# Kernel optimization log

Measured on AMD Instinct MI355X. Metric: run time of the kernel, lower is better.

The kernel has to match this reference:

```python
import jax, jax.numpy as jnp
import numpy as np

TEMPERATURE = 1.0


def setup_inputs() -> dict:
    key = jax.random.key(0)
    kq, kk, kv = jax.random.split(key, 3)
    shape = (2, 16, 2048, 64)  # B, H, L, D
    q = jax.random.normal(kq, shape, dtype=jnp.float32)
    k = jax.random.normal(kk, shape, dtype=jnp.float32)
    v = jax.random.normal(kv, shape, dtype=jnp.float32)
    return {"q": q, "k": k, "v": v}


def reference(q, k, v):
    # q, k, v: [B, H, L, D]
    L = q.shape[2]
    # scores: [B, H, L, L]; note: divided by temperature, NOT sqrt(D), per source
    scores = jnp.einsum("bhqd,bhkd->bhqk", q, k) / TEMPERATURE
    # causal mask: position j > i masked with -inf
    causal = jnp.tril(jnp.ones((L, L), dtype=bool))  # True = keep
    scores = jnp.where(causal, scores, -jnp.inf)
    attn = jax.nn.softmax(scores, axis=-1)
    out = jnp.einsum("bhqk,bhkd->bhqd", attn, v)
    return out
```

## Files before the change

### kernel.cpp

```cpp
#include <hip/hip_runtime.h>
#include <math.h>


typedef __attribute__((ext_vector_type(8))) _Float16 f16x8;
typedef __attribute__((ext_vector_type(4))) _Float16 f16x4;
typedef __attribute__((ext_vector_type(4))) float f32x4;
typedef unsigned short u16;
typedef __attribute__((ext_vector_type(8))) u16 u16x8;

constexpr int Lq = 2048;
constexpr int Dd = 64;
constexpr int KT = 64;
constexpr int BH = 32;

#define SWZB(row, bcol) ((((row) * 128) + (bcol)) ^ (((row) & 7) << 4))

#define GLOAD_LDS16(g, l)                                                     \
  __builtin_amdgcn_global_load_lds(                                           \
      (const __attribute__((address_space(1))) void*)(g),                     \
      (__attribute__((address_space(3))) void*)(l), 16, 0, 0)

static __device__ __forceinline__ u16 f2h(float x) {
  return __builtin_bit_cast(u16, (_Float16)x);
}

constexpr int PREP_KB = (BH * Lq * Dd) / (256 * 16);

__global__ __launch_bounds__(256)
void attn_prep(const float* __restrict__ K, const float* __restrict__ V,
               u16* __restrict__ Kh, u16* __restrict__ VTh) {
  const int b = blockIdx.x;
  const int tid = threadIdx.x;
  if (b < PREP_KB) {
    const size_t base = ((size_t)b * 256 + tid) * 16;
    const f32x4* src = reinterpret_cast<const f32x4*>(K + base);
    u16x8 o0, o1;
    #pragma unroll
    for (int i = 0; i < 2; ++i) {
      const f32x4 a = src[i];
      #pragma unroll
      for (int j = 0; j < 4; ++j) o0[i * 4 + j] = f2h(a[j]);
    }
    #pragma unroll
    for (int i = 0; i < 2; ++i) {
      const f32x4 a = src[2 + i];
      #pragma unroll
      for (int j = 0; j < 4; ++j) o1[i * 4 + j] = f2h(a[j]);
    }
    *reinterpret_cast<u16x8*>(Kh + base) = o0;
    *reinterpret_cast<u16x8*>(Kh + base + 8) = o1;
  } else {
    __shared__ u16 lt[64][66];
    const int vb = b - PREP_KB;
    const int h = vb >> 5, tt = vb & 31;
    const float* Vt = V + ((size_t)h * Lq + tt * 64) * Dd;
    const int r = tid & 63, dg = tid >> 6;
    #pragma unroll
    for (int i = 0; i < 4; ++i) {
      const f32x4 a = *reinterpret_cast<const f32x4*>(Vt + (size_t)r * Dd + dg * 16 + i * 4);
      #pragma unroll
      for (int j = 0; j < 2; ++j) {
        const unsigned two =
            (unsigned)f2h(a[2 * j]) | ((unsigned)f2h(a[2 * j + 1]) << 16);
        *reinterpret_cast<unsigned*>(&lt[r][dg * 16 + i * 4 + j * 2]) = two;
      }
    }
    __syncthreads();
    const int d = tid >> 2, kq = tid & 3;
    u16x8 w0, w1;
    #pragma unroll
    for (int j = 0; j < 8; ++j) w0[j] = lt[kq * 16 + j][d];
    #pragma unroll
    for (int j = 0; j < 8; ++j) w1[j] = lt[kq * 16 + 8 + j][d];
    u16* dst = VTh + ((size_t)h * Dd + d) * Lq + tt * 64 + kq * 16;
    *reinterpret_cast<u16x8*>(dst) = w0;
    *reinterpret_cast<u16x8*>(dst + 8) = w1;
  }
}

constexpr int THREADS = 512;
constexpr int CHUNK = 128;
constexpr int NCHUNK = Lq / CHUNK;
constexpr int PAIRS = NCHUNK / 2;

__global__ __launch_bounds__(THREADS)
void attn_main(const float* __restrict__ Q, float* __restrict__ O,
               const u16* __restrict__ Kh, const u16* __restrict__ VTh) {
  __shared__ char ks[2][8192];
  __shared__ char vt2[2][8192];
  __shared__ char pl[8][2048];

  const int tid  = threadIdx.x;
  const int lane = tid & 63;
  const int wv   = tid >> 6;
  const int l15  = lane & 15;
  const int g    = lane >> 4;

  const int bh = blockIdx.x / PAIRS;
  const int pr = blockIdx.x % PAIRS;
  const float* Qb = Q + (size_t)bh * Lq * Dd;
  float*       Ob = O + (size_t)bh * Lq * Dd;
  const u16*   Kb = Kh + (size_t)bh * Lq * Dd;
  const u16*   Vb = VTh + (size_t)bh * Dd * Lq;
  char* pw = pl[wv];

  const int lsw = lane ^ ((lane >> 3) & 7);
  const int r_ = lsw >> 3, s_ = lsw & 7;

  #pragma unroll 1
  for (int phase = 0; phase < 2; ++phase) {
    const int chunk = (phase == 0) ? pr : (NCHUNK - 1 - pr);
    const int row0  = chunk * CHUNK;
    const int T     = 2 * (chunk + 1);
    const int qrow  = row0 + wv * 16;
    const int tLast = qrow >> 6;

    f16x8 qf[2];
    #pragma unroll
    for (int kk = 0; kk < 2; ++kk) {
      const float* qp = Qb + (size_t)(qrow + l15) * Dd + kk * 32 + g * 8;
      const f32x4 a = *reinterpret_cast<const f32x4*>(qp);
      const f32x4 b = *reinterpret_cast<const f32x4*>(qp + 4);
      f16x8 q8;
      #pragma unroll
      for (int i = 0; i < 4; ++i) {
        q8[i]     = (_Float16)a[i];
        q8[i + 4] = (_Float16)b[i];
      }
      qf[kk] = q8;
    }

    float m[4], lsum[4];
    f32x4 o[4];
    #pragma unroll
    for (int r = 0; r < 4; ++r) { m[r] = -INFINITY; lsum[r] = 0.f; }
    #pragma unroll
    for (int nd = 0; nd < 4; ++nd) o[nd] = f32x4{0.f, 0.f, 0.f, 0.f};

    __syncthreads();
    GLOAD_LDS16(Kb + (size_t)(8 * wv) * Dd + lsw * 8, ks[0] + wv * 1024);
    GLOAD_LDS16(Vb + (size_t)(8 * wv + r_) * Lq + s_ * 8, vt2[0] + wv * 1024);

    int cur = 0;
    #pragma unroll 1
    for (int t = 0; t < T; ++t) {
      __syncthreads();
      if (t + 1 < T) {
        GLOAD_LDS16(Kb + (size_t)((t + 1) * KT + 8 * wv) * Dd + lsw * 8,
                    ks[cur ^ 1] + wv * 1024);
        GLOAD_LDS16(Vb + (size_t)(8 * wv + r_) * Lq + (t + 1) * KT + s_ * 8,
                    vt2[cur ^ 1] + wv * 1024);
      }
      if (t <= tLast) {
        const char* kb = ks[cur];
        const char* vb = vt2[cur];

        f32x4 s[4];
        #pragma unroll
        for (int n = 0; n < 4; ++n) s[n] = f32x4{0.f, 0.f, 0.f, 0.f};
        __builtin_amdgcn_s_setprio(1);
        #pragma unroll
        for (int kk = 0; kk < 2; ++kk) {
          #pragma unroll
          for (int n = 0; n < 4; ++n) {
            const f16x8 kf = *reinterpret_cast<const f16x8*>(
                kb + SWZB(n * 16 + l15, kk * 64 + g * 16));
            s[n] = __builtin_amdgcn_mfma_f32_16x16x32_f16(qf[kk], kf, s[n], 0, 0, 0);
          }
        }
        __builtin_amdgcn_s_setprio(0);

        if (t == tLast) {
          #pragma unroll
          for (int n = 0; n < 4; ++n) {
            const int key = t * KT + n * 16 + l15;
            #pragma unroll
            for (int r = 0; r < 4; ++r) {
              if (key > qrow + 4 * g + r) s[n][r] = -INFINITY;
            }
          }
        }

        float rmax[4], rsum[4], scale[4];
        #pragma unroll
        for (int r = 0; r < 4; ++r)
          rmax[r] = fmaxf(fmaxf(s[0][r], s[1][r]), fmaxf(s[2][r], s[3][r]));
        #pragma unroll
        for (int mk = 1; mk <= 8; mk <<= 1) {
          #pragma unroll
          for (int r = 0; r < 4; ++r)
            rmax[r] = fmaxf(rmax[r], __shfl_xor(rmax[r], mk));
        }
        #pragma unroll
        for (int r = 0; r < 4; ++r) {
          const float mn = fmaxf(m[r], rmax[r]);
          scale[r] = __expf(m[r] - mn);
          m[r] = mn;
        }
        #pragma unroll
        for (int n = 0; n < 4; ++n) {
          #pragma unroll
          for (int r = 0; r < 4; ++r) s[n][r] = __expf(s[n][r] - m[r]);
        }
        #pragma unroll
        for (int r = 0; r < 4; ++r)
          rsum[r] = (s[0][r] + s[1][r]) + (s[2][r] + s[3][r]);
        #pragma unroll
        for (int mk = 1; mk <= 8; mk <<= 1) {
          #pragma unroll
          for (int r = 0; r < 4; ++r) rsum[r] += __shfl_xor(rsum[r], mk);
        }
        #pragma unroll
        for (int r = 0; r < 4; ++r) lsum[r] = lsum[r] * scale[r] + rsum[r];
        #pragma unroll
        for (int nd = 0; nd < 4; ++nd) {
          #pragma unroll
          for (int r = 0; r < 4; ++r) o[nd][r] *= scale[r];
        }

        #pragma unroll
        for (int n = 0; n < 4; ++n) {
          #pragma unroll
          for (int r = 0; r < 4; ++r) {
            *reinterpret_cast<_Float16*>(
                pw + SWZB(4 * g + r, (n * 16 + l15) * 2)) = (_Float16)s[n][r];
          }
        }
        asm volatile("s_waitcnt lgkmcnt(0)" ::: "memory");
        __builtin_amdgcn_sched_barrier(0);

        __builtin_amdgcn_s_setprio(1);
        #pragma unroll
        for (int kblk = 0; kblk < 2; ++kblk) {
          const f16x8 pf = *reinterpret_cast<const f16x8*>(
              pw + SWZB(l15, kblk * 64 + g * 16));
          #pragma unroll
          for (int nd = 0; nd < 4; ++nd) {
            const f16x8 vf = *reinterpret_cast<const f16x8*>(
                vb + SWZB(nd * 16 + l15, kblk * 64 + g * 16));
            o[nd] = __builtin_amdgcn_mfma_f32_16x16x32_f16(pf, vf, o[nd], 0, 0, 0);
          }
        }
        __builtin_amdgcn_s_setprio(0);
      }
      cur ^= 1;
    }

    float inv[4];
    #pragma unroll
    for (int r = 0; r < 4; ++r) inv[r] = 1.f / lsum[r];
    #pragma unroll
    for (int nd = 0; nd < 4; ++nd) {
      #pragma unroll
      for (int r = 0; r < 4; ++r) {
        Ob[(size_t)(qrow + 4 * g + r) * Dd + nd * 16 + l15] = o[nd][r] * inv[r];
      }
    }
  }
}

__global__ __launch_bounds__(256)
void causal_attn_fb(const float* __restrict__ Q, const float* __restrict__ K,
                    const float* __restrict__ V, float* __restrict__ O) {
  __shared__ char ks[2][KT * 128];
  __shared__ char vt[2][Dd * 128];
  __shared__ char pl[4][16 * 128];
  const int tid = threadIdx.x, lane = tid & 63, wv = tid >> 6;
  const int l15 = lane & 15, g = lane >> 4;
  const int kg = tid & 15, dq = tid >> 4;
  const int bh = blockIdx.x / 16, pr = blockIdx.x % 16;
  const size_t base = (size_t)bh * Lq * Dd;
  const float* Qb = Q + base; const float* Kb = K + base;
  const float* Vb = V + base; float* Ob = O + base;
  char* pw = pl[wv];
  #pragma unroll 1
  for (int phase = 0; phase < 2; ++phase) {
    const int chunk = (phase == 0) ? pr : (31 - pr);
    const int row0 = chunk * 64, T = chunk + 1, qrow = row0 + wv * 16;
    f16x8 qf[2];
    #pragma unroll
    for (int kk = 0; kk < 2; ++kk) {
      const float* qp = Qb + (size_t)(qrow + l15) * Dd + kk * 32 + g * 8;
      const f32x4 a = *reinterpret_cast<const f32x4*>(qp);
      const f32x4 b = *reinterpret_cast<const f32x4*>(qp + 4);
      f16x8 q8;
      #pragma unroll
      for (int i = 0; i < 4; ++i) { q8[i] = (_Float16)a[i]; q8[i+4] = (_Float16)b[i]; }
      qf[kk] = q8;
    }
    float m[4], lsum[4]; f32x4 o[4];
    #pragma unroll
    for (int r = 0; r < 4; ++r) { m[r] = -INFINITY; lsum[r] = 0.f; }
    #pragma unroll
    for (int nd = 0; nd < 4; ++nd) o[nd] = f32x4{0.f, 0.f, 0.f, 0.f};
    {
      f32x4 kreg[4], vreg[4];
      #pragma unroll
      for (int i = 0; i < 4; ++i) {
        const int c = tid + i * 256;
        kreg[i] = *reinterpret_cast<const f32x4*>(Kb + (size_t)(c >> 4) * Dd + (c & 15) * 4);
      }
      #pragma unroll
      for (int c = 0; c < 4; ++c)
        vreg[c] = *reinterpret_cast<const f32x4*>(Vb + (size_t)(kg * 4 + c) * Dd + dq * 4);
      __syncthreads();
      #pragma unroll
      for (int i = 0; i < 4; ++i) {
        const int c = tid + i * 256;
        f16x4 h;
        #pragma unroll
        for (int j = 0; j < 4; ++j) h[j] = (_Float16)kreg[i][j];
        *reinterpret_cast<f16x4*>(ks[0] + SWZB(c >> 4, (c & 15) * 8)) = h;
      }
      #pragma unroll
      for (int j = 0; j < 4; ++j) {
        f16x4 h;
        #pragma unroll
        for (int c = 0; c < 4; ++c) h[c] = (_Float16)vreg[c][j];
        *reinterpret_cast<f16x4*>(vt[0] + SWZB(dq * 4 + j, kg * 8)) = h;
      }
    }
    int cur = 0;
    #pragma unroll 1
    for (int t = 0; t < T; ++t) {
      __syncthreads();
      const char* kb = ks[cur]; const char* vb = vt[cur];
      f32x4 kreg[4], vreg[4];
      const bool pfn = (t + 1 < T);
      if (pfn) {
        const float* Kt = Kb + (size_t)(t + 1) * KT * Dd;
        const float* Vt = Vb + (size_t)(t + 1) * KT * Dd;
        #pragma unroll
        for (int i = 0; i < 4; ++i) {
          const int c = tid + i * 256;
          kreg[i] = *reinterpret_cast<const f32x4*>(Kt + (size_t)(c >> 4) * Dd + (c & 15) * 4);
        }
        #pragma unroll
        for (int c = 0; c < 4; ++c)
          vreg[c] = *reinterpret_cast<const f32x4*>(Vt + (size_t)(kg * 4 + c) * Dd + dq * 4);
      }
      f32x4 s[4];
      #pragma unroll
      for (int n = 0; n < 4; ++n) s[n] = f32x4{0.f, 0.f, 0.f, 0.f};
      #pragma unroll
      for (int kk = 0; kk < 2; ++kk) {
        #pragma unroll
        for (int n = 0; n < 4; ++n) {
          const f16x8 kf = *reinterpret_cast<const f16x8*>(kb + SWZB(n * 16 + l15, kk * 64 + g * 16));
          s[n] = __builtin_amdgcn_mfma_f32_16x16x32_f16(qf[kk], kf, s[n], 0, 0, 0);
        }
      }
      if (t == T - 1) {
        #pragma unroll
        for (int n = 0; n < 4; ++n) {
          const int key = t * KT + n * 16 + l15;
          #pragma unroll
          for (int r = 0; r < 4; ++r)
            if (key > qrow + 4 * g + r) s[n][r] = -INFINITY;
        }
      }
      float rmax[4], rsum[4], scale[4];
      #pragma unroll
      for (int r = 0; r < 4; ++r)
        rmax[r] = fmaxf(fmaxf(s[0][r], s[1][r]), fmaxf(s[2][r], s[3][r]));
      #pragma unroll
      for (int mk = 1; mk <= 8; mk <<= 1) {
        #pragma unroll
        for (int r = 0; r < 4; ++r) rmax[r] = fmaxf(rmax[r], __shfl_xor(rmax[r], mk));
      }
      #pragma unroll
      for (int r = 0; r < 4; ++r) {
        const float mn = fmaxf(m[r], rmax[r]);
        scale[r] = __expf(m[r] - mn); m[r] = mn;
      }
      #pragma unroll
      for (int n = 0; n < 4; ++n) {
        #pragma unroll
        for (int r = 0; r < 4; ++r) s[n][r] = __expf(s[n][r] - m[r]);
      }
      #pragma unroll
      for (int r = 0; r < 4; ++r) rsum[r] = (s[0][r] + s[1][r]) + (s[2][r] + s[3][r]);
      #pragma unroll
      for (int mk = 1; mk <= 8; mk <<= 1) {
        #pragma unroll
        for (int r = 0; r < 4; ++r) rsum[r] += __shfl_xor(rsum[r], mk);
      }
      #pragma unroll
      for (int r = 0; r < 4; ++r) lsum[r] = lsum[r] * scale[r] + rsum[r];
      #pragma unroll
      for (int nd = 0; nd < 4; ++nd) {
        #pragma unroll
        for (int r = 0; r < 4; ++r) o[nd][r] *= scale[r];
      }
      #pragma unroll
      for (int n = 0; n < 4; ++n) {
        #pragma unroll
        for (int r = 0; r < 4; ++r)
          *reinterpret_cast<_Float16*>(pw + SWZB(4 * g + r, (n * 16 + l15) * 2)) = (_Float16)s[n][r];
      }
      asm volatile("s_waitcnt lgkmcnt(0)" ::: "memory");
      __builtin_amdgcn_sched_barrier(0);
      #pragma unroll
      for (int kblk = 0; kblk < 2; ++kblk) {
        const f16x8 pf = *reinterpret_cast<const f16x8*>(pw + SWZB(l15, kblk * 64 + g * 16));
        #pragma unroll
        for (int nd = 0; nd < 4; ++nd) {
          const f16x8 vf = *reinterpret_cast<const f16x8*>(vb + SWZB(nd * 16 + l15, kblk * 64 + g * 16));
          o[nd] = __builtin_amdgcn_mfma_f32_16x16x32_f16(pf, vf, o[nd], 0, 0, 0);
        }
      }
      if (pfn) {
        char* kn = ks[cur ^ 1]; char* vn = vt[cur ^ 1];
        #pragma unroll
        for (int i = 0; i < 4; ++i) {
          const int c = tid + i * 256;
          f16x4 h;
          #pragma unroll
          for (int j = 0; j < 4; ++j) h[j] = (_Float16)kreg[i][j];
          *reinterpret_cast<f16x4*>(kn + SWZB(c >> 4, (c & 15) * 8)) = h;
        }
        #pragma unroll
        for (int j = 0; j < 4; ++j) {
          f16x4 h;
          #pragma unroll
          for (int c = 0; c < 4; ++c) h[c] = (_Float16)vreg[c][j];
          *reinterpret_cast<f16x4*>(vn + SWZB(dq * 4 + j, kg * 8)) = h;
        }
      }
      cur ^= 1;
    }
    float inv[4];
    #pragma unroll
    for (int r = 0; r < 4; ++r) inv[r] = 1.f / lsum[r];
    #pragma unroll
    for (int nd = 0; nd < 4; ++nd) {
      #pragma unroll
      for (int r = 0; r < 4; ++r)
        Ob[(size_t)(qrow + 4 * g + r) * Dd + nd * 16 + l15] = o[nd][r] * inv[r];
    }
  }
}

extern "C" void kernel_launch(void* const* d_in, const int* in_sizes, int n_in,
                              void* d_out, int out_size, void* d_ws, size_t ws_size,
                              hipStream_t stream) {
  const float* q = (const float*)d_in[0];
  const float* k = (const float*)d_in[1];
  const float* v = (const float*)d_in[2];
  float* o = (float*)d_out;
  const size_t elems = (size_t)BH * Lq * Dd;
  const size_t need = elems * 2 * 2;
  if (ws_size >= need) {
    u16* Kh = (u16*)d_ws;
    u16* VTh = Kh + elems;
    attn_prep<<<dim3(2 * PREP_KB), dim3(256), 0, stream>>>(k, v, Kh, VTh);
    attn_main<<<dim3(BH * PAIRS), dim3(THREADS), 0, stream>>>(q, o, Kh, VTh);
  } else {
    causal_attn_fb<<<dim3(BH * 16), dim3(256), 0, stream>>>(q, k, v, o);
  }
  (void)in_sizes; (void)n_in; (void)out_size;
}
```

Measured before the change: 84.19 us.

## Halve query chunk to 64 rows with 4 waves, add lazy rescale and block swizzle

Shrinks the workgroup to 256 threads and query chunks to 64 rows, so each chunk matches exactly one key tile on the diagonal and no wave sits idle on tiles beyond its causal limit. This doubles the block count to improve load balance and occupancy. Each wave now loads two 16-byte segments per tile so the K/V staging still covers the 64-key tile. It adds a lazy softmax rescale that only updates m, lsum and o when a wave-wide row max grows by more than 8, skipping most rescale multiplies. It also remaps block IDs with a swizzle, presumably for L2 locality. The risks are more K/V traffic per query row, since each tile is reloaded per 64-row chunk, and a larger fp16 P range under the lazy threshold, which could cost accuracy.

Result: faster. 81.53 us (-3.2%).

```diff
diff --git a/kernel.cpp b/kernel.cpp
--- a/kernel.cpp
+++ b/kernel.cpp
@@ -78,8 +78,8 @@
   }
 }
 
-constexpr int THREADS = 512;
-constexpr int CHUNK = 128;
+constexpr int THREADS = 256;
+constexpr int CHUNK = 64;
 constexpr int NCHUNK = Lq / CHUNK;
 constexpr int PAIRS = NCHUNK / 2;
 
@@ -88,7 +88,7 @@
                const u16* __restrict__ Kh, const u16* __restrict__ VTh) {
   __shared__ char ks[2][8192];
   __shared__ char vt2[2][8192];
-  __shared__ char pl[8][2048];
+  __shared__ char pl[4][2048];
 
   const int tid  = threadIdx.x;
   const int lane = tid & 63;
@@ -96,8 +96,11 @@
   const int l15  = lane & 15;
   const int g    = lane >> 4;
 
-  const int bh = blockIdx.x / PAIRS;
-  const int pr = blockIdx.x % PAIRS;
+  const int bid = blockIdx.x;
+  const int swz = (bid & 7) * 64 + (bid >> 3);
+  const int bh = swz / PAIRS;
+  const int pr = swz % PAIRS;
+
   const float* Qb = Q + (size_t)bh * Lq * Dd;
   float*       Ob = O + (size_t)bh * Lq * Dd;
   const u16*   Kb = Kh + (size_t)bh * Lq * Dd;
@@ -111,9 +114,8 @@
   for (int phase = 0; phase < 2; ++phase) {
     const int chunk = (phase == 0) ? pr : (NCHUNK - 1 - pr);
     const int row0  = chunk * CHUNK;
-    const int T     = 2 * (chunk + 1);
+    const int T     = chunk + 1;
     const int qrow  = row0 + wv * 16;
-    const int tLast = qrow >> 6;
 
     f16x8 qf[2];
     #pragma unroll
@@ -138,111 +140,123 @@
     for (int nd = 0; nd < 4; ++nd) o[nd] = f32x4{0.f, 0.f, 0.f, 0.f};
 
     __syncthreads();
-    GLOAD_LDS16(Kb + (size_t)(8 * wv) * Dd + lsw * 8, ks[0] + wv * 1024);
-    GLOAD_LDS16(Vb + (size_t)(8 * wv + r_) * Lq + s_ * 8, vt2[0] + wv * 1024);
+    #pragma unroll
+    for (int i = 0; i < 2; ++i) {
+      GLOAD_LDS16(Kb + (size_t)(16 * wv + 8 * i + r_) * Dd + s_ * 8,
+                  ks[0] + wv * 2048 + i * 1024);
+      GLOAD_LDS16(Vb + (size_t)(16 * wv + 8 * i + r_) * Lq + s_ * 8,
+                  vt2[0] + wv * 2048 + i * 1024);
+    }
 
     int cur = 0;
     #pragma unroll 1
     for (int t = 0; t < T; ++t) {
       __syncthreads();
       if (t + 1 < T) {
-        GLOAD_LDS16(Kb + (size_t)((t + 1) * KT + 8 * wv) * Dd + lsw * 8,
-                    ks[cur ^ 1] + wv * 1024);
-        GLOAD_LDS16(Vb + (size_t)(8 * wv + r_) * Lq + (t + 1) * KT + s_ * 8,
-                    vt2[cur ^ 1] + wv * 1024);
-      }
-      if (t <= tLast) {
-        const char* kb = ks[cur];
-        const char* vb = vt2[cur];
-
-        f32x4 s[4];
-        #pragma unroll
-        for (int n = 0; n < 4; ++n) s[n] = f32x4{0.f, 0.f, 0.f, 0.f};
-        __builtin_amdgcn_s_setprio(1);
-        #pragma unroll
-        for (int kk = 0; kk < 2; ++kk) {
+        #pragma unroll
+        for (int i = 0; i < 2; ++i) {
+          GLOAD_LDS16(Kb + (size_t)((t + 1) * KT + 16 * wv + 8 * i + r_) * Dd + s_ * 8,
+                      ks[cur ^ 1] + wv * 2048 + i * 1024);
+          GLOAD_LDS16(Vb + (size_t)(16 * wv + 8 * i + r_) * Lq + (t + 1) * KT + s_ * 8,
+                      vt2[cur ^ 1] + wv * 2048 + i * 1024);
+        }
+      }
+      const char* kb = ks[cur];
+      const char* vb = vt2[cur];
+
+      f32x4 s[4];
+      #pragma unroll
+      for (int n = 0; n < 4; ++n) s[n] = f32x4{0.f, 0.f, 0.f, 0.f};
+      __builtin_amdgcn_s_setprio(1);
+      #pragma unroll
+      for (int kk = 0; kk < 2; ++kk) {
+        #pragma unroll
+        for (int n = 0; n < 4; ++n) {
+          const f16x8 kf = *reinterpret_cast<const f16x8*>(
+              kb + SWZB(n * 16 + l15, kk * 64 + g * 16));
+          s[n] = __builtin_amdgcn_mfma_f32_16x16x32_f16(qf[kk], kf, s[n], 0, 0, 0);
+        }
+      }
+      __builtin_amdgcn_s_setprio(0);
+
+      if (t == T - 1) {
+        #pragma unroll
+        for (int n = 0; n < 4; ++n) {
+          const int key = t * KT + n * 16 + l15;
           #pragma unroll
-          for (int n = 0; n < 4; ++n) {
-            const f16x8 kf = *reinterpret_cast<const f16x8*>(
-                kb + SWZB(n * 16 + l15, kk * 64 + g * 16));
-            s[n] = __builtin_amdgcn_mfma_f32_16x16x32_f16(qf[kk], kf, s[n], 0, 0, 0);
+          for (int r = 0; r < 4; ++r) {
+            if (key > qrow + 4 * g + r) s[n][r] = -INFINITY;
           }
         }
-        __builtin_amdgcn_s_setprio(0);
-
-        if (t == tLast) {
-          #pragma unroll
-          for (int n = 0; n < 4; ++n) {
-            const int key = t * KT + n * 16 + l15;
-            #pragma unroll
-            for (int r = 0; r < 4; ++r) {
-              if (key > qrow + 4 * g + r) s[n][r] = -INFINITY;
-            }
-          }
-        }
-
-        float rmax[4], rsum[4], scale[4];
+      }
+
+      float rmax[4], rsum[4], scale[4];
+      #pragma unroll
+      for (int r = 0; r < 4; ++r)
+        rmax[r] = fmaxf(fmaxf(s[0][r], s[1][r]), fmaxf(s[2][r], s[3][r]));
+      #pragma unroll
+      for (int mk = 1; mk <= 8; mk <<= 1) {
         #pragma unroll
         for (int r = 0; r < 4; ++r)
-          rmax[r] = fmaxf(fmaxf(s[0][r], s[1][r]), fmaxf(s[2][r], s[3][r]));
-        #pragma unroll
-        for (int mk = 1; mk <= 8; mk <<= 1) {
-          #pragma unroll
-          for (int r = 0; r < 4; ++r)
-            rmax[r] = fmaxf(rmax[r], __shfl_xor(rmax[r], mk));
-        }
+          rmax[r] = fmaxf(rmax[r], __shfl_xor(rmax[r], mk));
+      }
+      bool grow = false;
+      #pragma unroll
+      for (int r = 0; r < 4; ++r) grow |= (rmax[r] > m[r] + 8.f);
+      if (__any(grow)) {
         #pragma unroll
         for (int r = 0; r < 4; ++r) {
           const float mn = fmaxf(m[r], rmax[r]);
           scale[r] = __expf(m[r] - mn);
           m[r] = mn;
-        }
-        #pragma unroll
-        for (int n = 0; n < 4; ++n) {
-          #pragma unroll
-          for (int r = 0; r < 4; ++r) s[n][r] = __expf(s[n][r] - m[r]);
-        }
-        #pragma unroll
-        for (int r = 0; r < 4; ++r)
-          rsum[r] = (s[0][r] + s[1][r]) + (s[2][r] + s[3][r]);
-        #pragma unroll
-        for (int mk = 1; mk <= 8; mk <<= 1) {
-          #pragma unroll
-          for (int r = 0; r < 4; ++r) rsum[r] += __shfl_xor(rsum[r], mk);
-        }
-        #pragma unroll
-        for (int r = 0; r < 4; ++r) lsum[r] = lsum[r] * scale[r] + rsum[r];
+          lsum[r] *= scale[r];
+        }
         #pragma unroll
         for (int nd = 0; nd < 4; ++nd) {
           #pragma unroll
           for (int r = 0; r < 4; ++r) o[nd][r] *= scale[r];
         }
-
-        #pragma unroll
-        for (int n = 0; n < 4; ++n) {
-          #pragma unroll
-          for (int r = 0; r < 4; ++r) {
-            *reinterpret_cast<_Float16*>(
-                pw + SWZB(4 * g + r, (n * 16 + l15) * 2)) = (_Float16)s[n][r];
-          }
-        }
-        asm volatile("s_waitcnt lgkmcnt(0)" ::: "memory");
-        __builtin_amdgcn_sched_barrier(0);
-
-        __builtin_amdgcn_s_setprio(1);
-        #pragma unroll
-        for (int kblk = 0; kblk < 2; ++kblk) {
-          const f16x8 pf = *reinterpret_cast<const f16x8*>(
-              pw + SWZB(l15, kblk * 64 + g * 16));
-          #pragma unroll
-          for (int nd = 0; nd < 4; ++nd) {
-            const f16x8 vf = *reinterpret_cast<const f16x8*>(
-                vb + SWZB(nd * 16 + l15, kblk * 64 + g * 16));
-            o[nd] = __builtin_amdgcn_mfma_f32_16x16x32_f16(pf, vf, o[nd], 0, 0, 0);
-          }
-        }
-        __builtin_amdgcn_s_setprio(0);
-      }
+      }
+      #pragma unroll
+      for (int n = 0; n < 4; ++n) {
+        #pragma unroll
+        for (int r = 0; r < 4; ++r) s[n][r] = __expf(s[n][r] - m[r]);
+      }
+      #pragma unroll
+      for (int r = 0; r < 4; ++r)
+        rsum[r] = (s[0][r] + s[1][r]) + (s[2][r] + s[3][r]);
+      #pragma unroll
+      for (int mk = 1; mk <= 8; mk <<= 1) {
+        #pragma unroll
+        for (int r = 0; r < 4; ++r) rsum[r] += __shfl_xor(rsum[r], mk);
+      }
+      #pragma unroll
+      for (int r = 0; r < 4; ++r) lsum[r] += rsum[r];
+
+      #pragma unroll
+      for (int n = 0; n < 4; ++n) {
+        #pragma unroll
+        for (int r = 0; r < 4; ++r) {
+          *reinterpret_cast<_Float16*>(
+              pw + SWZB(4 * g + r, (n * 16 + l15) * 2)) = (_Float16)s[n][r];
+        }
+      }
+      asm volatile("s_waitcnt lgkmcnt(0)" ::: "memory");
+      __builtin_amdgcn_sched_barrier(0);
+
+      __builtin_amdgcn_s_setprio(1);
+      #pragma unroll
+      for (int kblk = 0; kblk < 2; ++kblk) {
+        const f16x8 pf = *reinterpret_cast<const f16x8*>(
+            pw + SWZB(l15, kblk * 64 + g * 16));
+        #pragma unroll
+        for (int nd = 0; nd < 4; ++nd) {
+          const f16x8 vf = *reinterpret_cast<const f16x8*>(
+              vb + SWZB(nd * 16 + l15, kblk * 64 + g * 16));
+          o[nd] = __builtin_amdgcn_mfma_f32_16x16x32_f16(pf, vf, o[nd], 0, 0, 0);
+        }
+      }
+      __builtin_amdgcn_s_setprio(0);
       cur ^= 1;
     }
 
```

## Rewrite main attention kernel with 32x32 MFMA, register-resident P, lazy rescale

Applied to the files above, without the earlier changes.

Restructures the main kernel so each 128-thread block handles one 64-row query chunk, with two waves of 32 rows each. Both matmuls now use the 32x32x16 MFMA, computing S transposed so the probabilities are repacked into the A operand via lane shuffles instead of an LDS round trip. The online-softmax rescale is skipped unless the row max grows by more than 8, and fully masked diagonal sub-tiles are skipped. The aim is to cut LDS traffic, synchronisation and softmax overhead. The trade-offs are smaller blocks, a new chunk-to-block ordering for load balance, and per-row max tracking that relies on the threshold staying numerically safe.

Result: faster. 78.71 us, median of 3 (-6.5%).

```diff
diff --git a/kernel.cpp b/kernel.cpp
--- a/kernel.cpp
+++ b/kernel.cpp
@@ -4,9 +4,13 @@
 
 typedef __attribute__((ext_vector_type(8))) _Float16 f16x8;
 typedef __attribute__((ext_vector_type(4))) _Float16 f16x4;
+typedef __attribute__((ext_vector_type(2))) _Float16 f16x2;
 typedef __attribute__((ext_vector_type(4))) float f32x4;
+typedef __attribute__((ext_vector_type(16))) float f32x16;
 typedef unsigned short u16;
+typedef unsigned int u32;
 typedef __attribute__((ext_vector_type(8))) u16 u16x8;
+typedef __attribute__((ext_vector_type(4))) u32 u32x4;
 
 constexpr int Lq = 2048;
 constexpr int Dd = 64;
@@ -78,184 +82,203 @@
   }
 }
 
-constexpr int THREADS = 512;
-constexpr int CHUNK = 128;
-constexpr int NCHUNK = Lq / CHUNK;
-constexpr int PAIRS = NCHUNK / 2;
-
-__global__ __launch_bounds__(THREADS)
+__global__ __launch_bounds__(128)
 void attn_main(const float* __restrict__ Q, float* __restrict__ O,
                const u16* __restrict__ Kh, const u16* __restrict__ VTh) {
   __shared__ char ks[2][8192];
   __shared__ char vt2[2][8192];
-  __shared__ char pl[8][2048];
+  __shared__ float bc[2][32];
 
   const int tid  = threadIdx.x;
   const int lane = tid & 63;
   const int wv   = tid >> 6;
-  const int l15  = lane & 15;
-  const int g    = lane >> 4;
-
-  const int bh = blockIdx.x / PAIRS;
-  const int pr = blockIdx.x % PAIRS;
-  const float* Qb = Q + (size_t)bh * Lq * Dd;
-  float*       Ob = O + (size_t)bh * Lq * Dd;
-  const u16*   Kb = Kh + (size_t)bh * Lq * Dd;
-  const u16*   Vb = VTh + (size_t)bh * Dd * Lq;
-  char* pw = pl[wv];
-
-  const int lsw = lane ^ ((lane >> 3) & 7);
-  const int r_ = lsw >> 3, s_ = lsw & 7;
-
+  const int l31  = lane & 31;
+  const int hi   = lane >> 5;
+
+  const int b = blockIdx.x;
+  const int j = b >> 8;
+  const int i = b & 255;
+  const int h = i >> 3;
+  const int p = i & 7;
+  const int chunk = (j == 0) ? p : (j == 1) ? (31 - p) : (j == 2) ? (p + 8) : (23 - p);
+
+  const float* Qb = Q + (size_t)h * Lq * Dd;
+  float*       Ob = O + (size_t)h * Lq * Dd;
+  const u16*   Kb = Kh + (size_t)h * Lq * Dd;
+  const u16*   Vb = VTh + (size_t)h * Dd * Lq;
+
+  const int row0 = chunk * 64;
+  const int T    = chunk + 1;
+  const int qrow = row0 + wv * 32;
+
+  f16x8 qf[4];
+  #pragma unroll
+  for (int kc = 0; kc < 4; ++kc) {
+    const float* qp = Qb + (size_t)(qrow + l31) * Dd + kc * 16 + hi * 8;
+    const f32x4 a = *reinterpret_cast<const f32x4*>(qp);
+    const f32x4 c = *reinterpret_cast<const f32x4*>(qp + 4);
+    f16x8 q8;
+    #pragma unroll
+    for (int e = 0; e < 4; ++e) {
+      q8[e]     = (_Float16)a[e];
+      q8[e + 4] = (_Float16)c[e];
+    }
+    qf[kc] = q8;
+  }
+
+  float m = -INFINITY, lsum = 0.f;
+  f32x16 o0, o1;
+  #pragma unroll
+  for (int e = 0; e < 16; ++e) { o0[e] = 0.f; o1[e] = 0.f; }
+
+  const int rr = lane >> 3;
+  const int c0 = (lane & 7) ^ rr;
+
+  #pragma unroll
+  for (int it = 0; it < 4; ++it) {
+    const int row = wv * 32 + it * 8 + rr;
+    GLOAD_LDS16(Kb + (size_t)row * Dd + c0 * 8,
+                &ks[0][wv * 4096 + it * 1024 + lane * 16]);
+    GLOAD_LDS16(Vb + (size_t)row * Lq + c0 * 8,
+                &vt2[0][wv * 4096 + it * 1024 + lane * 16]);
+  }
+
+  int cur = 0;
   #pragma unroll 1
-  for (int phase = 0; phase < 2; ++phase) {
-    const int chunk = (phase == 0) ? pr : (NCHUNK - 1 - pr);
-    const int row0  = chunk * CHUNK;
-    const int T     = 2 * (chunk + 1);
-    const int qrow  = row0 + wv * 16;
-    const int tLast = qrow >> 6;
-
-    f16x8 qf[2];
-    #pragma unroll
-    for (int kk = 0; kk < 2; ++kk) {
-      const float* qp = Qb + (size_t)(qrow + l15) * Dd + kk * 32 + g * 8;
-      const f32x4 a = *reinterpret_cast<const f32x4*>(qp);
-      const f32x4 b = *reinterpret_cast<const f32x4*>(qp + 4);
-      f16x8 q8;
-      #pragma unroll
-      for (int i = 0; i < 4; ++i) {
-        q8[i]     = (_Float16)a[i];
-        q8[i + 4] = (_Float16)b[i];
-      }
-      qf[kk] = q8;
-    }
-
-    float m[4], lsum[4];
-    f32x4 o[4];
-    #pragma unroll
-    for (int r = 0; r < 4; ++r) { m[r] = -INFINITY; lsum[r] = 0.f; }
-    #pragma unroll
-    for (int nd = 0; nd < 4; ++nd) o[nd] = f32x4{0.f, 0.f, 0.f, 0.f};
-
+  for (int t = 0; t < T; ++t) {
     __syncthreads();
-    GLOAD_LDS16(Kb + (size_t)(8 * wv) * Dd + lsw * 8, ks[0] + wv * 1024);
-    GLOAD_LDS16(Vb + (size_t)(8 * wv + r_) * Lq + s_ * 8, vt2[0] + wv * 1024);
-
-    int cur = 0;
-    #pragma unroll 1
-    for (int t = 0; t < T; ++t) {
-      __syncthreads();
-      if (t + 1 < T) {
-        GLOAD_LDS16(Kb + (size_t)((t + 1) * KT + 8 * wv) * Dd + lsw * 8,
-                    ks[cur ^ 1] + wv * 1024);
-        GLOAD_LDS16(Vb + (size_t)(8 * wv + r_) * Lq + (t + 1) * KT + s_ * 8,
-                    vt2[cur ^ 1] + wv * 1024);
-      }
-      if (t <= tLast) {
-        const char* kb = ks[cur];
-        const char* vb = vt2[cur];
-
-        f32x4 s[4];
-        #pragma unroll
-        for (int n = 0; n < 4; ++n) s[n] = f32x4{0.f, 0.f, 0.f, 0.f};
+    if (t + 1 < T) {
+      #pragma unroll
+      for (int it = 0; it < 4; ++it) {
+        const int row = wv * 32 + it * 8 + rr;
+        GLOAD_LDS16(Kb + (size_t)((t + 1) * KT + row) * Dd + c0 * 8,
+                    &ks[cur ^ 1][wv * 4096 + it * 1024 + lane * 16]);
+        GLOAD_LDS16(Vb + (size_t)row * Lq + (t + 1) * KT + c0 * 8,
+                    &vt2[cur ^ 1][wv * 4096 + it * 1024 + lane * 16]);
+      }
+    }
+    const char* kb = ks[cur];
+    const char* vb = vt2[cur];
+    const bool last  = (t == T - 1);
+    const bool have1 = !(last && wv == 0);
+
+    f32x16 st0, st1;
+    #pragma unroll
+    for (int e = 0; e < 16; ++e) { st0[e] = 0.f; st1[e] = 0.f; }
+    __builtin_amdgcn_s_setprio(1);
+    #pragma unroll
+    for (int kc = 0; kc < 4; ++kc) {
+      const f16x8 kf = *reinterpret_cast<const f16x8*>(
+          kb + SWZB(l31, kc * 32 + hi * 16));
+      st0 = __builtin_amdgcn_mfma_f32_32x32x16_f16(kf, qf[kc], st0, 0, 0, 0);
+    }
+    if (have1) {
+      #pragma unroll
+      for (int kc = 0; kc < 4; ++kc) {
+        const f16x8 kf = *reinterpret_cast<const f16x8*>(
+            kb + SWZB(32 + l31, kc * 32 + hi * 16));
+        st1 = __builtin_amdgcn_mfma_f32_32x32x16_f16(kf, qf[kc], st1, 0, 0, 0);
+      }
+    }
+    __builtin_amdgcn_s_setprio(0);
+
+    if (last) {
+      #pragma unroll
+      for (int r = 0; r < 16; ++r) {
+        const int crow = (r & 3) + 8 * (r >> 2) + 4 * hi;
+        if (wv == 0) { if (crow > l31) st0[r] = -INFINITY; }
+        else         { if (crow > l31) st1[r] = -INFINITY; }
+      }
+    }
+
+    float pm = st0[0];
+    #pragma unroll
+    for (int r = 1; r < 16; ++r) pm = fmaxf(pm, st0[r]);
+    if (have1) {
+      #pragma unroll
+      for (int r = 0; r < 16; ++r) pm = fmaxf(pm, st1[r]);
+    }
+    pm = fmaxf(pm, __shfl_xor(pm, 32));
+
+    if (__any(pm > m + 8.f)) {
+      const float mn = fmaxf(m, pm);
+      const float sc = __expf(m - mn);
+      m = mn;
+      lsum *= sc;
+      if (hi == 0) bc[wv][l31] = sc;
+      const f32x4 s0 = *reinterpret_cast<const f32x4*>(&bc[wv][4 * hi]);
+      const f32x4 s1 = *reinterpret_cast<const f32x4*>(&bc[wv][8 + 4 * hi]);
+      const f32x4 s2 = *reinterpret_cast<const f32x4*>(&bc[wv][16 + 4 * hi]);
+      const f32x4 s3 = *reinterpret_cast<const f32x4*>(&bc[wv][24 + 4 * hi]);
+      #pragma unroll
+      for (int r = 0; r < 16; ++r) {
+        const float fac = (r < 4) ? s0[r & 3] : (r < 8) ? s1[r & 3]
+                        : (r < 12) ? s2[r & 3] : s3[r & 3];
+        o0[r] *= fac;
+        o1[r] *= fac;
+      }
+    }
+
+    float rs = 0.f;
+    #pragma unroll
+    for (int r = 0; r < 16; ++r) { st0[r] = __expf(st0[r] - m); rs += st0[r]; }
+    if (have1) {
+      #pragma unroll
+      for (int r = 0; r < 16; ++r) { st1[r] = __expf(st1[r] - m); rs += st1[r]; }
+    }
+    rs += __shfl_xor(rs, 32);
+    lsum += rs;
+
+    #pragma unroll
+    for (int ksub = 0; ksub < 2; ++ksub) {
+      if (ksub == 1 && !have1) break;
+      const f32x16& st = (ksub == 0) ? st0 : st1;
+      #pragma unroll
+      for (int ks2 = 0; ks2 < 2; ++ks2) {
+        const u32 pe0 = __builtin_bit_cast(u32,
+            __builtin_amdgcn_cvt_pkrtz(st[8 * ks2 + 0], st[8 * ks2 + 1]));
+        const u32 pe1 = __builtin_bit_cast(u32,
+            __builtin_amdgcn_cvt_pkrtz(st[8 * ks2 + 2], st[8 * ks2 + 3]));
+        const u32 po0 = __builtin_bit_cast(u32,
+            __builtin_amdgcn_cvt_pkrtz(st[8 * ks2 + 4], st[8 * ks2 + 5]));
+        const u32 po1 = __builtin_bit_cast(u32,
+            __builtin_amdgcn_cvt_pkrtz(st[8 * ks2 + 6], st[8 * ks2 + 7]));
+        const u32 re0 = __shfl_xor(pe0, 32);
+        const u32 re1 = __shfl_xor(pe1, 32);
+        const u32 ro0 = __shfl_xor(po0, 32);
+        const u32 ro1 = __shfl_xor(po1, 32);
+        u32x4 w;
+        w[0] = hi ? ro0 : pe0;
+        w[1] = hi ? ro1 : pe1;
+        w[2] = hi ? po0 : re0;
+        w[3] = hi ? po1 : re1;
+        const f16x8 pa = __builtin_bit_cast(f16x8, w);
+        const int cb = ksub * 64 + ks2 * 32 + hi * 16;
+        const f16x8 v0 = *reinterpret_cast<const f16x8*>(vb + SWZB(l31, cb));
+        const f16x8 v1 = *reinterpret_cast<const f16x8*>(vb + SWZB(32 + l31, cb));
         __builtin_amdgcn_s_setprio(1);
-        #pragma unroll
-        for (int kk = 0; kk < 2; ++kk) {
-          #pragma unroll
-          for (int n = 0; n < 4; ++n) {
-            const f16x8 kf = *reinterpret_cast<const f16x8*>(
-                kb + SWZB(n * 16 + l15, kk * 64 + g * 16));
-            s[n] = __builtin_amdgcn_mfma_f32_16x16x32_f16(qf[kk], kf, s[n], 0, 0, 0);
-          }
-        }
+        o0 = __builtin_amdgcn_mfma_f32_32x32x16_f16(pa, v0, o0, 0, 0, 0);
+        o1 = __builtin_amdgcn_mfma_f32_32x32x16_f16(pa, v1, o1, 0, 0, 0);
         __builtin_amdgcn_s_setprio(0);
-
-        if (t == tLast) {
-          #pragma unroll
-          for (int n = 0; n < 4; ++n) {
-            const int key = t * KT + n * 16 + l15;
-            #pragma unroll
-            for (int r = 0; r < 4; ++r) {
-              if (key > qrow + 4 * g + r) s[n][r] = -INFINITY;
-            }
-          }
-        }
-
-        float rmax[4], rsum[4], scale[4];
-        #pragma unroll
-        for (int r = 0; r < 4; ++r)
-          rmax[r] = fmaxf(fmaxf(s[0][r], s[1][r]), fmaxf(s[2][r], s[3][r]));
-        #pragma unroll
-        for (int mk = 1; mk <= 8; mk <<= 1) {
-          #pragma unroll
-          for (int r = 0; r < 4; ++r)
-            rmax[r] = fmaxf(rmax[r], __shfl_xor(rmax[r], mk));
-        }
-        #pragma unroll
-        for (int r = 0; r < 4; ++r) {
-          const float mn = fmaxf(m[r], rmax[r]);
-          scale[r] = __expf(m[r] - mn);
-          m[r] = mn;
-        }
-        #pragma unroll
-        for (int n = 0; n < 4; ++n) {
-          #pragma unroll
-          for (int r = 0; r < 4; ++r) s[n][r] = __expf(s[n][r] - m[r]);
-        }
-        #pragma unroll
-        for (int r = 0; r < 4; ++r)
-          rsum[r] = (s[0][r] + s[1][r]) + (s[2][r] + s[3][r]);
-        #pragma unroll
-        for (int mk = 1; mk <= 8; mk <<= 1) {
-          #pragma unroll
-          for (int r = 0; r < 4; ++r) rsum[r] += __shfl_xor(rsum[r], mk);
-        }
-        #pragma unroll
-        for (int r = 0; r < 4; ++r) lsum[r] = lsum[r] * scale[r] + rsum[r];
-        #pragma unroll
-        for (int nd = 0; nd < 4; ++nd) {
-          #pragma unroll
-          for (int r = 0; r < 4; ++r) o[nd][r] *= scale[r];
-        }
-
-        #pragma unroll
-        for (int n = 0; n < 4; ++n) {
-          #pragma unroll
-          for (int r = 0; r < 4; ++r) {
-            *reinterpret_cast<_Float16*>(
-                pw + SWZB(4 * g + r, (n * 16 + l15) * 2)) = (_Float16)s[n][r];
-          }
-        }
-        asm volatile("s_waitcnt lgkmcnt(0)" ::: "memory");
-        __builtin_amdgcn_sched_barrier(0);
-
-        __builtin_amdgcn_s_setprio(1);
-        #pragma unroll
-        for (int kblk = 0; kblk < 2; ++kblk) {
-          const f16x8 pf = *reinterpret_cast<const f16x8*>(
-              pw + SWZB(l15, kblk * 64 + g * 16));
-          #pragma unroll
-          for (int nd = 0; nd < 4; ++nd) {
-            const f16x8 vf = *reinterpret_cast<const f16x8*>(
-                vb + SWZB(nd * 16 + l15, kblk * 64 + g * 16));
-            o[nd] = __builtin_amdgcn_mfma_f32_16x16x32_f16(pf, vf, o[nd], 0, 0, 0);
-          }
-        }
-        __builtin_amdgcn_s_setprio(0);
-      }
-      cur ^= 1;
-    }
-
-    float inv[4];
-    #pragma unroll
-    for (int r = 0; r < 4; ++r) inv[r] = 1.f / lsum[r];
-    #pragma unroll
-    for (int nd = 0; nd < 4; ++nd) {
-      #pragma unroll
-      for (int r = 0; r < 4; ++r) {
-        Ob[(size_t)(qrow + 4 * g + r) * Dd + nd * 16 + l15] = o[nd][r] * inv[r];
-      }
-    }
+      }
+    }
+    cur ^= 1;
+  }
+
+  const float inv = 1.f / lsum;
+  if (hi == 0) bc[wv][l31] = inv;
+  const f32x4 i0 = *reinterpret_cast<const f32x4*>(&bc[wv][4 * hi]);
+  const f32x4 i1 = *reinterpret_cast<const f32x4*>(&bc[wv][8 + 4 * hi]);
+  const f32x4 i2 = *reinterpret_cast<const f32x4*>(&bc[wv][16 + 4 * hi]);
+  const f32x4 i3 = *reinterpret_cast<const f32x4*>(&bc[wv][24 + 4 * hi]);
+  #pragma unroll
+  for (int r = 0; r < 16; ++r) {
+    const int crow = (r & 3) + 8 * (r >> 2) + 4 * hi;
+    const float fac = (r < 4) ? i0[r & 3] : (r < 8) ? i1[r & 3]
+                    : (r < 12) ? i2[r & 3] : i3[r & 3];
+    float* op = Ob + (size_t)(qrow + crow) * Dd + l31;
+    op[0]  = o0[r] * fac;
+    op[32] = o1[r] * fac;
   }
 }
 
@@ -307,17 +330,17 @@
       #pragma unroll
       for (int i = 0; i < 4; ++i) {
         const int c = tid + i * 256;
-        f16x4 h;
-        #pragma unroll
-        for (int j = 0; j < 4; ++j) h[j] = (_Float16)kreg[i][j];
-        *reinterpret_cast<f16x4*>(ks[0] + SWZB(c >> 4, (c & 15) * 8)) = h;
-      }
-      #pragma unroll
-      for (int j = 0; j < 4; ++j) {
-        f16x4 h;
-        #pragma unroll
-        for (int c = 0; c < 4; ++c) h[c] = (_Float16)vreg[c][j];
-        *reinterpret_cast<f16x4*>(vt[0] + SWZB(dq * 4 + j, kg * 8)) = h;
+        f16x4 hh;
+        #pragma unroll
+        for (int jj = 0; jj < 4; ++jj) hh[jj] = (_Float16)kreg[i][jj];
+        *reinterpret_cast<f16x4*>(ks[0] + SWZB(c >> 4, (c & 15) * 8)) = hh;
+      }
+      #pragma unroll
+      for (int jj = 0; jj < 4; ++jj) {
+        f16x4 hh;
+        #pragma unroll
+        for (int c = 0; c < 4; ++c) hh[c] = (_Float16)vreg[c][jj];
+        *reinterpret_cast<f16x4*>(vt[0] + SWZB(dq * 4 + jj, kg * 8)) = hh;
       }
     }
     int cur = 0;
@@ -414,17 +437,17 @@
         #pragma unroll
         for (int i = 0; i < 4; ++i) {
           const int c = tid + i * 256;
-          f16x4 h;
+          f16x4 hh;
           #pragma unroll
-          for (int j = 0; j < 4; ++j) h[j] = (_Float16)kreg[i][j];
-          *reinterpret_cast<f16x4*>(kn + SWZB(c >> 4, (c & 15) * 8)) = h;
-        }
-        #pragma unroll
-        for (int j = 0; j < 4; ++j) {
-          f16x4 h;
+          for (int jj = 0; jj < 4; ++jj) hh[jj] = (_Float16)kreg[i][jj];
+          *reinterpret_cast<f16x4*>(kn + SWZB(c >> 4, (c & 15) * 8)) = hh;
+        }
+        #pragma unroll
+        for (int jj = 0; jj < 4; ++jj) {
+          f16x4 hh;
           #pragma unroll
-          for (int c = 0; c < 4; ++c) h[c] = (_Float16)vreg[c][j];
-          *reinterpret_cast<f16x4*>(vn + SWZB(dq * 4 + j, kg * 8)) = h;
+          for (int c = 0; c < 4; ++c) hh[c] = (_Float16)vreg[c][jj];
+          *reinterpret_cast<f16x4*>(vn + SWZB(dq * 4 + jj, kg * 8)) = hh;
         }
       }
       cur ^= 1;
@@ -454,7 +477,7 @@
     u16* Kh = (u16*)d_ws;
     u16* VTh = Kh + elems;
     attn_prep<<<dim3(2 * PREP_KB), dim3(256), 0, stream>>>(k, v, Kh, VTh);
-    attn_main<<<dim3(BH * PAIRS), dim3(THREADS), 0, stream>>>(q, o, Kh, VTh);
+    attn_main<<<dim3(BH * 32), dim3(128), 0, stream>>>(q, o, Kh, VTh);
   } else {
     causal_attn_fb<<<dim3(BH * 16), dim3(256), 0, stream>>>(q, k, v, o);
   }
```
